# Kernel optimization log

Measured on AMD Instinct MI355X. Metric: run time of the kernel, lower is better.

## Reference

```python
import jax, jax.numpy as jnp
import numpy as np

MARGIN = 0.3
EPS = 1e-6      # torch F.pairwise_distance eps used inside TripletMarginLoss
BIG = 1000000.0  # same sentinel as original code


def setup_inputs() -> dict:
    key = jax.random.key(0)
    k1, k2 = jax.random.split(key)
    embeddings = jax.random.normal(k1, (4096, 2048), dtype=jnp.float32)
    labels = jax.random.randint(k2, (4096,), 0, 128)  # 128 identities -> ~32 samples each
    return {"embeddings": embeddings, "labels": labels}


def _batch_hard_triplet_loss(emb, labels):
    B = emb.shape[0]
    # pairwise euclidean distances (torch.cdist p=2)
    sq = jnp.sum(emb * emb, axis=1)                      # [B]
    d2 = sq[:, None] + sq[None, :] - 2.0 * (emb @ emb.T)  # [B,B]
    dists = jnp.sqrt(jnp.maximum(d2, 0.0))

    same = labels[:, None] == labels[None, :]            # [B,B] bool
    eye = jnp.eye(B, dtype=bool)
    pos_mask = same & ~eye

    # hard positive: argmax over same-label (self set to -1, others-with-diff-label masked to 0*d -> use -1 uniformly for non-positives, matching dists*mask_pos with diag=-1 since dists>=0)
    pos_d = jnp.where(pos_mask, dists, -1.0)
    hard_pos = jnp.argmax(pos_d, axis=1)                 # [B]
    # hard negative: argmin over different-label (same-label gets +1e6 like original)
    neg_d = jnp.where(same, dists + BIG, dists)
    hard_neg = jnp.argmin(neg_d, axis=1)                 # [B]

    # valid anchors: at least one positive (other than self) and one negative
    valid = (jnp.sum(pos_mask, axis=1) > 0) & (jnp.sum(~same, axis=1) > 0)

    # TripletMarginLoss recomputes distances with eps added to the difference
    dp = jnp.linalg.norm(emb - emb[hard_pos] + EPS, axis=1)
    dn = jnp.linalg.norm(emb - emb[hard_neg] + EPS, axis=1)
    per = jnp.maximum(dp - dn + MARGIN, 0.0)

    cnt = jnp.sum(valid)
    total = jnp.sum(jnp.where(valid, per, 0.0))
    return jnp.where(cnt > 0, total / jnp.maximum(cnt, 1).astype(per.dtype), 0.0)


def reference(embeddings, labels):
    return _batch_hard_triplet_loss(embeddings, labels)
```

## Files before the change

kernel.cpp:

```cpp
#include <hip/hip_runtime.h>
#include <stdint.h>

#define B 4096
#define D 2048
#define BK 128
#define NITER (D / BK)
#define BM 64
#define BN 128

typedef unsigned long long ull;
typedef float f32x4 __attribute__((ext_vector_type(4)));
typedef long v2l __attribute__((ext_vector_type(2)));

#define SENT_P 0x00000000FFFFFFFFull
#define SENT_N (~0ull)

__device__ __forceinline__ void async_copy16(const unsigned char* g, unsigned char* l) {
  __builtin_amdgcn_global_load_lds(
      (const __attribute__((address_space(1))) unsigned int*)g,
      (__attribute__((address_space(3))) unsigned int*)l,
      16, 0, 0);
}

__global__ void k_convert_sq(const float* __restrict__ emb,
                             unsigned char* __restrict__ embq,
                             float* __restrict__ sq,
                             float* __restrict__ rs,
                             ull* __restrict__ bp,
                             ull* __restrict__ bn,
                             float* __restrict__ red_sum,
                             int* __restrict__ red_cnt,
                             int* __restrict__ red_done) {
  const int row = blockIdx.x, t = threadIdx.x;
  const float4* src = (const float4*)(emb + (size_t)row * D);
  float4 v0 = src[2 * t], v1 = src[2 * t + 1];
  float s = v0.x * v0.x + v0.y * v0.y + v0.z * v0.z + v0.w * v0.w
          + v1.x * v1.x + v1.y * v1.y + v1.z * v1.z + v1.w * v1.w;
  float sm = v0.x + v0.y + v0.z + v0.w + v1.x + v1.y + v1.z + v1.w;

  unsigned w0 = __builtin_amdgcn_cvt_pk_fp8_f32(v0.x, v0.y, 0, false);
  w0 = __builtin_amdgcn_cvt_pk_fp8_f32(v0.z, v0.w, w0, true);
  unsigned w1 = __builtin_amdgcn_cvt_pk_fp8_f32(v1.x, v1.y, 0, false);
  w1 = __builtin_amdgcn_cvt_pk_fp8_f32(v1.z, v1.w, w1, true);
  uint2 o; o.x = w0; o.y = w1;
  const int pos = ((t >> 4) << 7) | ((t & 3) << 5) | (((t >> 2) & 3) << 3);
  *(uint2*)(embq + (size_t)row * D + pos) = o;

  for (int off = 32; off; off >>= 1) {
    s  += __shfl_down(s, off, 64);
    sm += __shfl_down(sm, off, 64);
  }
  __shared__ float ps[4], pm[4];
  int lane = t & 63, wave = t >> 6;
  if (lane == 0) { ps[wave] = s; pm[wave] = sm; }
  __syncthreads();
  if (t == 0) {
    sq[row] = ps[0] + ps[1] + ps[2] + ps[3];
    rs[row] = pm[0] + pm[1] + pm[2] + pm[3];
    bp[row] = SENT_P;
    bn[row] = SENT_N;
    if (row == 0) { *red_sum = 0.0f; *red_cnt = 0; *red_done = 0; }
  }
}

__launch_bounds__(128, 3)
__global__ void k_gemm_select(const unsigned char* __restrict__ embq,
                              const float* __restrict__ sq,
                              const int* __restrict__ labels,
                              ull* __restrict__ best_pos,
                              ull* __restrict__ best_neg) {
  __shared__ __align__(16) unsigned char ldsA[BM * BK];
  __shared__ __align__(16) unsigned char ldsB[BN * BK];

  int rem = blockIdx.x, p = 0;
  while (rem >= 2 * (32 - p)) { rem -= 2 * (32 - p); ++p; }
  int by = 2 * p;
  int c = 32 - p;
  if (rem >= c) { by += 1; rem -= c; }
  const int bx = p + rem;

  const int tid  = threadIdx.x;
  const int lane = tid & 63;
  const int wave = tid >> 6;
  const int q = lane >> 4, m15 = lane & 15;
  const int ibase = by * BM, jbase = bx * BN;

  int aoff[2][4], boff[2][4];
#pragma unroll
  for (int sh = 0; sh < 2; ++sh) {
#pragma unroll
    for (int g = 0; g < 4; ++g) {
      int ra = g * 16 + m15;
      aoff[sh][g] = ra * BK + (((q * 2 + sh) ^ (ra & 7)) * 16);
      int rb = wave * 64 + g * 16 + m15;
      boff[sh][g] = rb * BK + (((q * 2 + sh) ^ (rb & 7)) * 16);
    }
  }

  const int srow = lane >> 3;
  const int slot = lane & 7;
  size_t agoff[4], bgoff[8];
  int lasta[4], lastb[8];
#pragma unroll
  for (int pp = 0; pp < 4; ++pp) {
    int r0  = wave * 32 + pp * 8;
    int row = r0 + srow;
    agoff[pp] = (size_t)(ibase + row) * D + (slot ^ (row & 7)) * 16;
    lasta[pp] = r0 * BK;
  }
#pragma unroll
  for (int pp = 0; pp < 8; ++pp) {
    int r0  = wave * 64 + pp * 8;
    int row = r0 + srow;
    bgoff[pp] = (size_t)(jbase + row) * D + (slot ^ (row & 7)) * 16;
    lastb[pp] = r0 * BK;
  }

  f32x4 acc[4][4];
  const f32x4 z = {0.f, 0.f, 0.f, 0.f};
#pragma unroll
  for (int a = 0; a < 4; ++a)
#pragma unroll
    for (int b = 0; b < 4; ++b) acc[a][b] = z;

  for (int kb = 0; kb < D; kb += BK) {
    __syncthreads();
#pragma unroll
    for (int pp = 0; pp < 4; ++pp)
      async_copy16(embq + agoff[pp] + kb, &ldsA[lasta[pp]]);
#pragma unroll
    for (int pp = 0; pp < 8; ++pp)
      async_copy16(embq + bgoff[pp] + kb, &ldsB[lastb[pp]]);
    __syncthreads();

#pragma unroll
    for (int sh = 0; sh < 2; ++sh) {
      v2l af[4], bf[4];
#pragma unroll
      for (int g = 0; g < 4; ++g) af[g] = *(const v2l*)&ldsA[aoff[sh][g]];
#pragma unroll
      for (int g = 0; g < 4; ++g) bf[g] = *(const v2l*)&ldsB[boff[sh][g]];
#pragma unroll
      for (int mi = 0; mi < 4; ++mi)
#pragma unroll
        for (int ni = 0; ni < 4; ++ni)
          acc[mi][ni] = __builtin_amdgcn_mfma_f32_16x16x32_fp8_fp8(
              af[mi][0], bf[ni][0], acc[mi][ni], 0, 0, 0);
#pragma unroll
      for (int mi = 0; mi < 4; ++mi)
#pragma unroll
        for (int ni = 0; ni < 4; ++ni)
          acc[mi][ni] = __builtin_amdgcn_mfma_f32_16x16x32_fp8_fp8(
              af[mi][1], bf[ni][1], acc[mi][ni], 0, 0, 0);
    }
  }

  float sqj[4];
  int labj[4];
#pragma unroll
  for (int ni = 0; ni < 4; ++ni) {
    int jj = jbase + wave * 64 + ni * 16 + m15;
    sqj[ni] = sq[jj];
    labj[ni] = labels[jj];
  }

  ull colBp[4], colBn[4];
#pragma unroll
  for (int ni = 0; ni < 4; ++ni) { colBp[ni] = SENT_P; colBn[ni] = SENT_N; }

#pragma unroll
  for (int mi = 0; mi < 4; ++mi) {
#pragma unroll
    for (int r = 0; r < 4; ++r) {
      const int i = ibase + mi * 16 + q * 4 + r;
      const float si = sq[i];
      const int li = labels[i];
      ull bp = SENT_P;
      ull bn = SENT_N;
#pragma unroll
      for (int ni = 0; ni < 4; ++ni) {
        int jj = jbase + wave * 64 + ni * 16 + m15;
        if (jj > i) {
          float dot = acc[mi][ni][r];
          float d2 = si + sqj[ni] - 2.0f * dot;
          float dist = sqrtf(fmaxf(d2, 0.0f));
          ull pv = ((ull)__float_as_uint(dist)) << 32;
          if (labj[ni] == li) {
            ull cr = pv | (unsigned)(~jj);
            bp = bp > cr ? bp : cr;
            ull cc = pv | (unsigned)(~i);
            colBp[ni] = colBp[ni] > cc ? colBp[ni] : cc;
          } else {
            ull cr = pv | (unsigned)jj;
            bn = bn < cr ? bn : cr;
            ull cc = pv | (unsigned)i;
            colBn[ni] = colBn[ni] < cc ? colBn[ni] : cc;
          }
        }
      }
#pragma unroll
      for (int off = 1; off <= 8; off <<= 1) {
        ull op = __shfl_xor(bp, off, 64);
        ull on = __shfl_xor(bn, off, 64);
        bp = bp > op ? bp : op;
        bn = bn < on ? bn : on;
      }
      if (m15 == 0) {
        if (bp != SENT_P) atomicMax(&best_pos[i], bp);
        if (bn != SENT_N) atomicMin(&best_neg[i], bn);
      }
    }
  }

#pragma unroll
  for (int ni = 0; ni < 4; ++ni) {
    ull cp = colBp[ni], cn = colBn[ni];
#pragma unroll
    for (int off = 16; off <= 32; off <<= 1) {
      ull op = __shfl_xor(cp, off, 64);
      ull on = __shfl_xor(cn, off, 64);
      cp = cp > op ? cp : op;
      cn = cn < on ? cn : on;
    }
    if (q == 0) {
      int j = jbase + wave * 64 + ni * 16 + m15;
      if (cp != SENT_P) atomicMax(&best_pos[j], cp);
      if (cn != SENT_N) atomicMin(&best_neg[j], cn);
    }
  }
}

__global__ void k_loss_final(const ull* __restrict__ best_pos,
                             const ull* __restrict__ best_neg,
                             const float* __restrict__ rs,
                             float* __restrict__ red_sum,
                             int* __restrict__ red_cnt,
                             int* __restrict__ red_done,
                             float* __restrict__ out) {
  const int i = blockIdx.x * 256 + threadIdx.x;
  float per = 0.0f;
  int v = 0;
  ull bp = best_pos[i], bn = best_neg[i];
  if (bp != SENT_P && bn != SENT_N) {
    unsigned pRaw = ~(unsigned)bp;
    unsigned nRaw = (unsigned)bn;
    int pi = pRaw < (unsigned)B ? (int)pRaw : 0;
    int ni = nRaw < (unsigned)B ? (int)nRaw : 0;
    float distp = __uint_as_float((unsigned)(bp >> 32));
    float distn = __uint_as_float((unsigned)(bn >> 32));
    float ri = rs[i];
    const float e = 1e-6f, de2 = (float)D * 1e-12f;
    float dp2 = distp * distp + 2.0f * e * (ri - rs[pi]) + de2;
    float dn2 = distn * distn + 2.0f * e * (ri - rs[ni]) + de2;
    float dp = sqrtf(fmaxf(dp2, 0.0f));
    float dn = sqrtf(fmaxf(dn2, 0.0f));
    per = fmaxf(dp - dn + 0.3f, 0.0f);
    v = 1;
  }
  for (int off = 32; off; off >>= 1) {
    per += __shfl_down(per, off, 64);
    v   += __shfl_down(v, off, 64);
  }
  __shared__ float pps[4];
  __shared__ int pvs[4];
  int lane = threadIdx.x & 63, wave = threadIdx.x >> 6;
  if (lane == 0) { pps[wave] = per; pvs[wave] = v; }
  __syncthreads();
  if (threadIdx.x == 0) {
    float t = pps[0] + pps[1] + pps[2] + pps[3];
    int cv = pvs[0] + pvs[1] + pvs[2] + pvs[3];
    atomicAdd(red_sum, t);
    atomicAdd(red_cnt, cv);
    __threadfence();
    int old = atomicAdd(red_done, 1);
    if (old == (int)gridDim.x - 1) {
      float s = atomicAdd(red_sum, 0.0f);
      int cc = atomicAdd(red_cnt, 0);
      out[0] = cc > 0 ? s / (float)cc : 0.0f;
    }
  }
}

extern "C" void kernel_launch(void* const* d_in, const int* in_sizes, int n_in,
                              void* d_out, int out_size, void* d_ws, size_t ws_size,
                              hipStream_t stream) {
  const float* emb = (const float*)d_in[0];
  const int* labels = (const int*)d_in[1];
  float* out = (float*)d_out;
  char* ws = (char*)d_ws;

  const size_t off_embq = 0;
  const size_t off_sq   = off_embq + (size_t)B * D;
  const size_t off_rs   = off_sq + (size_t)B * 4;
  const size_t off_bp   = off_rs + (size_t)B * 4;
  const size_t off_bn   = off_bp + (size_t)B * 8;
  const size_t off_red  = off_bn + (size_t)B * 8;

  unsigned char* embq = (unsigned char*)(ws + off_embq);
  float* sq   = (float*)(ws + off_sq);
  float* rs   = (float*)(ws + off_rs);
  ull* bp     = (ull*)(ws + off_bp);
  ull* bn     = (ull*)(ws + off_bn);
  float* red_sum = (float*)(ws + off_red);
  int* red_cnt   = (int*)(ws + off_red + 4);
  int* red_done  = (int*)(ws + off_red + 8);

  hipLaunchKernelGGL(k_convert_sq, dim3(B), dim3(256), 0, stream,
                     emb, embq, sq, rs, bp, bn, red_sum, red_cnt, red_done);
  hipLaunchKernelGGL(k_gemm_select, dim3(1056), dim3(128), 0, stream,
                     embq, sq, labels, bp, bn);
  hipLaunchKernelGGL(k_loss_final, dim3(B / 256), dim3(256), 0, stream,
                     bp, bn, rs, red_sum, red_cnt, red_done, out);
}
```

Before: 129.6 us.

## Double-buffer LDS tiles and split GEMM block across four waves

```diff
diff --git a/kernel.cpp b/kernel.cpp
--- a/kernel.cpp
+++ b/kernel.cpp
@@ -63,14 +63,14 @@
   }
 }
 
-__launch_bounds__(128, 3)
+__launch_bounds__(256, 3)
 __global__ void k_gemm_select(const unsigned char* __restrict__ embq,
                               const float* __restrict__ sq,
                               const int* __restrict__ labels,
                               ull* __restrict__ best_pos,
                               ull* __restrict__ best_neg) {
-  __shared__ __align__(16) unsigned char ldsA[BM * BK];
-  __shared__ __align__(16) unsigned char ldsB[BN * BK];
+  __shared__ __align__(16) unsigned char ldsA[2][BM * BK];
+  __shared__ __align__(16) unsigned char ldsB[2][BN * BK];
 
   int rem = blockIdx.x, p = 0;
   while (rem >= 2 * (32 - p)) { rem -= 2 * (32 - p); ++p; }
@@ -82,84 +82,101 @@
   const int tid  = threadIdx.x;
   const int lane = tid & 63;
   const int wave = tid >> 6;
+  const int wm = wave >> 1, wn = wave & 1;
   const int q = lane >> 4, m15 = lane & 15;
   const int ibase = by * BM, jbase = bx * BN;
 
-  int aoff[2][4], boff[2][4];
+  int aoff[2][2], boff[2][4];
 #pragma unroll
   for (int sh = 0; sh < 2; ++sh) {
 #pragma unroll
+    for (int g = 0; g < 2; ++g) {
+      int ra = wm * 32 + g * 16 + m15;
+      aoff[sh][g] = ra * BK + (((q * 2 + sh) ^ (ra & 7)) * 16);
+    }
+#pragma unroll
     for (int g = 0; g < 4; ++g) {
-      int ra = g * 16 + m15;
-      aoff[sh][g] = ra * BK + (((q * 2 + sh) ^ (ra & 7)) * 16);
-      int rb = wave * 64 + g * 16 + m15;
+      int rb = wn * 64 + g * 16 + m15;
       boff[sh][g] = rb * BK + (((q * 2 + sh) ^ (rb & 7)) * 16);
     }
   }
 
   const int srow = lane >> 3;
   const int slot = lane & 7;
-  size_t agoff[4], bgoff[8];
-  int lasta[4], lastb[8];
+  size_t agoff[2], bgoff[4];
+  int lasta[2], lastb[4];
+#pragma unroll
+  for (int pp = 0; pp < 2; ++pp) {
+    int r0  = wave * 16 + pp * 8;
+    int row = r0 + srow;
+    agoff[pp] = (size_t)(ibase + row) * D + (slot ^ (row & 7)) * 16;
+    lasta[pp] = r0 * BK;
+  }
 #pragma unroll
   for (int pp = 0; pp < 4; ++pp) {
     int r0  = wave * 32 + pp * 8;
     int row = r0 + srow;
-    agoff[pp] = (size_t)(ibase + row) * D + (slot ^ (row & 7)) * 16;
-    lasta[pp] = r0 * BK;
-  }
-#pragma unroll
-  for (int pp = 0; pp < 8; ++pp) {
-    int r0  = wave * 64 + pp * 8;
-    int row = r0 + srow;
     bgoff[pp] = (size_t)(jbase + row) * D + (slot ^ (row & 7)) * 16;
     lastb[pp] = r0 * BK;
   }
 
-  f32x4 acc[4][4];
+  f32x4 acc[2][4];
   const f32x4 z = {0.f, 0.f, 0.f, 0.f};
 #pragma unroll
-  for (int a = 0; a < 4; ++a)
+  for (int a = 0; a < 2; ++a)
 #pragma unroll
     for (int b = 0; b < 4; ++b) acc[a][b] = z;
 
-  for (int kb = 0; kb < D; kb += BK) {
-    __syncthreads();
+  auto stage = [&](int buf, int kb) {
+#pragma unroll
+    for (int pp = 0; pp < 2; ++pp)
+      async_copy16(embq + agoff[pp] + kb, &ldsA[buf][lasta[pp]]);
 #pragma unroll
     for (int pp = 0; pp < 4; ++pp)
-      async_copy16(embq + agoff[pp] + kb, &ldsA[lasta[pp]]);
-#pragma unroll
-    for (int pp = 0; pp < 8; ++pp)
-      async_copy16(embq + bgoff[pp] + kb, &ldsB[lastb[pp]]);
-    __syncthreads();
-
+      async_copy16(embq + bgoff[pp] + kb, &ldsB[buf][lastb[pp]]);
+  };
+
+  auto compute = [&](int buf) {
 #pragma unroll
     for (int sh = 0; sh < 2; ++sh) {
-      v2l af[4], bf[4];
-#pragma unroll
-      for (int g = 0; g < 4; ++g) af[g] = *(const v2l*)&ldsA[aoff[sh][g]];
-#pragma unroll
-      for (int g = 0; g < 4; ++g) bf[g] = *(const v2l*)&ldsB[boff[sh][g]];
-#pragma unroll
-      for (int mi = 0; mi < 4; ++mi)
+      v2l af[2], bf[4];
+#pragma unroll
+      for (int g = 0; g < 2; ++g) af[g] = *(const v2l*)&ldsA[buf][aoff[sh][g]];
+#pragma unroll
+      for (int g = 0; g < 4; ++g) bf[g] = *(const v2l*)&ldsB[buf][boff[sh][g]];
+#pragma unroll
+      for (int mi = 0; mi < 2; ++mi)
 #pragma unroll
         for (int ni = 0; ni < 4; ++ni)
           acc[mi][ni] = __builtin_amdgcn_mfma_f32_16x16x32_fp8_fp8(
               af[mi][0], bf[ni][0], acc[mi][ni], 0, 0, 0);
 #pragma unroll
-      for (int mi = 0; mi < 4; ++mi)
+      for (int mi = 0; mi < 2; ++mi)
 #pragma unroll
         for (int ni = 0; ni < 4; ++ni)
           acc[mi][ni] = __builtin_amdgcn_mfma_f32_16x16x32_fp8_fp8(
               af[mi][1], bf[ni][1], acc[mi][ni], 0, 0, 0);
     }
+  };
+
+  stage(0, 0);
+  asm volatile("s_waitcnt vmcnt(0)" ::: "memory");
+  __builtin_amdgcn_s_barrier();
+  asm volatile("" ::: "memory");
+
+  for (int t = 0; t < NITER; ++t) {
+    if (t + 1 < NITER) stage((t + 1) & 1, (t + 1) * BK);
+    compute(t & 1);
+    asm volatile("s_waitcnt vmcnt(0)" ::: "memory");
+    __builtin_amdgcn_s_barrier();
+    asm volatile("" ::: "memory");
   }
 
   float sqj[4];
   int labj[4];
 #pragma unroll
   for (int ni = 0; ni < 4; ++ni) {
-    int jj = jbase + wave * 64 + ni * 16 + m15;
+    int jj = jbase + wn * 64 + ni * 16 + m15;
     sqj[ni] = sq[jj];
     labj[ni] = labels[jj];
   }
@@ -169,17 +186,17 @@
   for (int ni = 0; ni < 4; ++ni) { colBp[ni] = SENT_P; colBn[ni] = SENT_N; }
 
 #pragma unroll
-  for (int mi = 0; mi < 4; ++mi) {
+  for (int mi = 0; mi < 2; ++mi) {
 #pragma unroll
     for (int r = 0; r < 4; ++r) {
-      const int i = ibase + mi * 16 + q * 4 + r;
+      const int i = ibase + wm * 32 + mi * 16 + q * 4 + r;
       const float si = sq[i];
       const int li = labels[i];
       ull bp = SENT_P;
       ull bn = SENT_N;
 #pragma unroll
       for (int ni = 0; ni < 4; ++ni) {
-        int jj = jbase + wave * 64 + ni * 16 + m15;
+        int jj = jbase + wn * 64 + ni * 16 + m15;
         if (jj > i) {
           float dot = acc[mi][ni][r];
           float d2 = si + sqj[ni] - 2.0f * dot;
@@ -223,7 +240,7 @@
       cn = cn < on ? cn : on;
     }
     if (q == 0) {
-      int j = jbase + wave * 64 + ni * 16 + m15;
+      int j = jbase + wn * 64 + ni * 16 + m15;
       if (cp != SENT_P) atomicMax(&best_pos[j], cp);
       if (cn != SENT_N) atomicMin(&best_neg[j], cn);
     }
@@ -307,7 +324,7 @@
 
   hipLaunchKernelGGL(k_convert_sq, dim3(B), dim3(256), 0, stream,
                      emb, embq, sq, rs, bp, bn, red_sum, red_cnt, red_done);
-  hipLaunchKernelGGL(k_gemm_select, dim3(1056), dim3(128), 0, stream,
+  hipLaunchKernelGGL(k_gemm_select, dim3(1056), dim3(256), 0, stream,
                      embq, sq, labels, bp, bn);
   hipLaunchKernelGGL(k_loss_final, dim3(B / 256), dim3(256), 0, stream,
                      bp, bn, rs, red_sum, red_cnt, red_done, out);
```

Result: slower. 135.6 us (+4.6%).
